# Kernel tuning notes

Measured on AMD Instinct MI355X. Metric: run time of the kernel, lower is better.

The kernel has to match this reference:

```python
import jax, jax.numpy as jnp
import numpy as np

B, T, C = 8, 1024, 1024
H, HKV = 16, 4
HD = C // H            # 64
G = H // HKV           # 4 (GQA group size)
CAP = 50.0
THETA = 10000.0
EPS = 1e-6


def _rope_tables(t, d, theta):
    inv_freq = 1.0 / (theta ** (jnp.arange(0, d, 2, dtype=jnp.float32) / d))
    pos = jnp.arange(t, dtype=jnp.float32)
    freqs = jnp.outer(pos, inv_freq)            # [T, d/2]
    return jnp.cos(freqs), jnp.sin(freqs)


def _rmsnorm(x, w):
    var = jnp.mean(x * x, axis=-1, keepdims=True)
    return x * jax.lax.rsqrt(var + EPS) * w


def _apply_rope(x, cos, sin):
    # x: [B, T, h, HD]; cos/sin: [T, HD/2]
    d = x.shape[-1] // 2
    x1, x2 = x[..., :d], x[..., d:]
    c = cos[None, :, None, :]
    s = sin[None, :, None, :]
    return jnp.concatenate([x1 * c + x2 * s, -x1 * s + x2 * c], axis=-1)


def setup_inputs() -> dict:
    key = jax.random.key(0)
    ks = jax.random.split(key, 6)
    std = 0.02
    x = jax.random.normal(ks[0], (B, T, C), dtype=jnp.float32)
    w_q = jax.random.normal(ks[1], (C, C), dtype=jnp.float32) * std
    w_kv = jax.random.normal(ks[2], (2 * C // G, C), dtype=jnp.float32) * std  # [512, 1024]
    w_c = jax.random.normal(ks[3], (C, C), dtype=jnp.float32) * std
    q_norm_w = jnp.ones((HD,), dtype=jnp.float32)
    k_norm_w = jnp.ones((HD,), dtype=jnp.float32)
    return {"x": x, "w_q": w_q, "w_kv": w_kv, "w_c": w_c,
            "q_norm_w": q_norm_w, "k_norm_w": k_norm_w}


def reference(x, w_q, w_kv, w_c, q_norm_w, k_norm_w):
    # projections (no bias)
    q = (x @ w_q.T).reshape(B, T, H, HD)
    kv = (x @ w_kv.T).reshape(B, T, 2, HKV, HD)
    k, v = kv[:, :, 0], kv[:, :, 1]            # [B, T, HKV, HD]

    # RMSNorm on q/k heads
    q = _rmsnorm(q, q_norm_w)
    k = _rmsnorm(k, k_norm_w)

    # RoPE (half-split rotation, as in apply_rotary_emb)
    cos, sin = _rope_tables(T, HD, THETA)
    q = _apply_rope(q, cos, sin)
    k = _apply_rope(k, cos, sin)

    # GQA layout: heads grouped over kv heads (equiv to repeat_interleave)
    q = q.transpose(0, 2, 1, 3).reshape(B, HKV, G, T, HD)   # [B, nkv, G, T, HD]
    k = k.transpose(0, 2, 1, 3)                             # [B, nkv, T, HD]
    v = v.transpose(0, 2, 1, 3)

    scale = 1.0 / jnp.sqrt(jnp.float32(HD))
    att = jnp.einsum('bngqd,bnkd->bngqk', q, k) * scale     # [B, nkv, G, T, T]
    att = CAP * jnp.tanh(att / CAP)                          # soft logit cap

    causal = jnp.arange(T)[:, None] >= jnp.arange(T)[None, :]  # [T, T]
    att = jnp.where(causal[None, None, None], att, -jnp.inf)
    att = jax.nn.softmax(att, axis=-1)

    y = jnp.einsum('bngqk,bnkd->bngqd', att, v)             # [B, nkv, G, T, HD]
    y = y.reshape(B, H, T, HD).transpose(0, 2, 1, 3).reshape(B, T, C)
    return y @ w_c.T
```

## Files before the change

kernel.cpp:

```cpp
#include <hip/hip_runtime.h>
#include <math.h>

#define BB 8
#define TT 1024
#define CC 1024
#define HH 16
#define HKV 4
#define HD 64
#define MM (BB*TT)
#define LOG2E 1.4426950408889634f

typedef __attribute__((ext_vector_type(8))) short bf16x8;
typedef __attribute__((ext_vector_type(4))) float f32x4;

__device__ __forceinline__ float b2f(unsigned short x){
    union{unsigned int i; float f;} u; u.i = ((unsigned int)x)<<16; return u.f;
}
__device__ __forceinline__ unsigned short f2b(float f){
    union{float f; unsigned int i;} u; u.f = f;
    unsigned int r = u.i + 0x7fffu + ((u.i>>16)&1u);
    return (unsigned short)(r>>16);
}

#define GLD16(gp, lp) __builtin_amdgcn_global_load_lds( \
    (__attribute__((address_space(1))) void*)(gp), \
    (__attribute__((address_space(3))) void*)(lp), 16, 0, 0)

__global__ __launch_bounds__(256) void cvt_all(const float* __restrict__ x,
                                               const float* __restrict__ w_q,
                                               const float* __restrict__ w_kv,
                                               const float* __restrict__ w_c,
                                               unsigned short* __restrict__ xb,
                                               unsigned short* __restrict__ wqkvb,
                                               unsigned short* __restrict__ wcb){
    int i = blockIdx.x*256 + threadIdx.x;
    const float* src; unsigned short* dst; int off;
    if (i < 2097152)      { src = x;    dst = xb;              off = i; }
    else if (i < 2359296) { src = w_q;  dst = wqkvb;           off = i - 2097152; }
    else if (i < 2490368) { src = w_kv; dst = wqkvb + 1048576; off = i - 2359296; }
    else                  { src = w_c;  dst = wcb;             off = i - 2490368; }
    float4 f = ((const float4*)src)[off];
    ushort4 o;
    o.x = f2b(f.x); o.y = f2b(f.y); o.z = f2b(f.z); o.w = f2b(f.w);
    ((ushort4*)dst)[off] = o;
}

template<int BF16OUT>
__global__ __launch_bounds__(256) void gemm_bt(const unsigned short* __restrict__ A,
                                               const unsigned short* __restrict__ Bt,
                                               void* __restrict__ Cc,
                                               int M, int N, int K){
    __shared__ __align__(16) unsigned short As[128*64];
    __shared__ __align__(16) unsigned short Bs[128*64];
    const int tid  = threadIdx.x;
    const int wid  = tid >> 6;
    const int lane = tid & 63;
    const int wm   = wid >> 1;
    const int wn   = wid & 1;
    const int l16  = lane & 15;
    const int quad = lane >> 4;

    int bm, bn;
    {
        int gx = gridDim.x;
        int p  = blockIdx.y * gx + blockIdx.x;
        int nb = gx * gridDim.y;
        int l  = (p & 7) * (nb >> 3) + (p >> 3);
        bn = (l % gx) * 128;
        bm = (l / gx) * 128;
    }

    const unsigned short* ga[4]; const unsigned short* gb[4];
    char* la[4]; char* lb[4];
    {
        int rbase = tid >> 3, c_lds = tid & 7;
        #pragma unroll
        for (int it = 0; it < 4; ++it){
            int row = it*32 + rbase;
            int cg  = c_lds ^ (row & 7);
            ga[it] = A  + (size_t)(bm+row)*K + cg*8;
            gb[it] = Bt + (size_t)(bn+row)*K + cg*8;
            la[it] = (char*)As + (size_t)(it*256 + tid)*16;
            lb[it] = (char*)Bs + (size_t)(it*256 + tid)*16;
        }
    }

    f32x4 acc[4][4] = {};

    for (int k0 = 0; k0 < K; k0 += 64){
        __syncthreads();
        #pragma unroll
        for (int it = 0; it < 4; ++it){
            GLD16(ga[it] + k0, la[it]);
            GLD16(gb[it] + k0, lb[it]);
        }
        __syncthreads();

        #pragma unroll
        for (int kh = 0; kh < 2; ++kh){
            bf16x8 af[4], bfr[4];
            #pragma unroll
            for (int i = 0; i < 4; ++i){
                int row = wm*64 + i*16 + l16;
                int ch  = (kh*4 + quad) ^ (row & 7);
                af[i] = *(const bf16x8*)(As + row*64 + ch*8);
            }
            #pragma unroll
            for (int j = 0; j < 4; ++j){
                int row = wn*64 + j*16 + l16;
                int ch  = (kh*4 + quad) ^ (row & 7);
                bfr[j] = *(const bf16x8*)(Bs + row*64 + ch*8);
            }
            #pragma unroll
            for (int i = 0; i < 4; ++i)
                #pragma unroll
                for (int j = 0; j < 4; ++j)
                    acc[i][j] = __builtin_amdgcn_mfma_f32_16x16x32_bf16(af[i], bfr[j], acc[i][j], 0, 0, 0);
        }
    }

    #pragma unroll
    for (int i = 0; i < 4; ++i){
        int row0 = wm*64 + i*16 + quad*4;
        #pragma unroll
        for (int j = 0; j < 4; ++j){
            int col = bn + wn*64 + j*16 + l16;
            #pragma unroll
            for (int r = 0; r < 4; ++r){
                if (BF16OUT)
                    ((unsigned short*)Cc)[(size_t)(bm + row0 + r)*N + col] = f2b(acc[i][j][r]);
                else
                    ((float*)Cc)[(size_t)(bm + row0 + r)*N + col] = acc[i][j][r];
            }
        }
    }
}

__global__ __launch_bounds__(256) void norm_rope_k(const unsigned short* __restrict__ QKVb,
                                                   const float* __restrict__ kw,
                                                   unsigned short* __restrict__ ka){
    int row  = blockIdx.x;
    int u    = threadIdx.x >> 6;
    int lane = threadIdx.x & 63;
    int b = row >> 10;
    int t = row & 1023;

    float val = b2f(QKVb[(size_t)row*1536 + 1024 + u*64 + lane]);

    float ss = val*val;
    #pragma unroll
    for (int off = 32; off > 0; off >>= 1) ss += __shfl_xor(ss, off, 64);
    float normed = val * rsqrtf(ss*(1.0f/64.0f) + 1e-6f) * kw[lane];

    int i = lane & 31;
    float freq = (float)t * exp2f(-(float)i * (13.287712379549449f/32.0f));
    float s, c;
    sincosf(freq, &s, &c);
    float other = __shfl_xor(normed, 32, 64);
    float outv = (lane < 32) ? (normed*c + other*s) : (-other*s + normed*c);

    ka[(((size_t)(b*HKV + u))*TT + t)*HD + lane] = f2b(outv);
}

__global__ __launch_bounds__(256) void vtrans(const unsigned short* __restrict__ QKVb,
                                              unsigned short* __restrict__ vat){
    __shared__ unsigned short tile[64][72];
    const int tid = threadIdx.x;
    const int tblk = blockIdx.x, n = blockIdx.y, b = blockIdx.z;
    #pragma unroll
    for (int it = 0; it < 2; ++it){
        int i = it*256 + tid;
        int r = i >> 3, c = i & 7;
        uint4 v = *(const uint4*)(QKVb + ((size_t)(b*TT + tblk*64 + r))*1536 + 1280 + n*64 + c*8);
        *(uint4*)(&tile[r][c*8]) = v;
    }
    __syncthreads();
    const int d = tid >> 2, tseg = tid & 3;
    unsigned short tmp[16];
    #pragma unroll
    for (int i = 0; i < 16; ++i) tmp[i] = tile[tseg*16 + i][d];
    size_t off = (((size_t)(b*HKV + n))*HD + d)*TT + tblk*64 + tseg*16;
    *(uint4*)(vat + off)     = *(const uint4*)tmp;
    *(uint4*)(vat + off + 8) = *(const uint4*)(tmp + 8);
}

__global__ __launch_bounds__(512, 4) void attn_mfma(const unsigned short* __restrict__ QKVb,
                                                    const unsigned short* __restrict__ ka,
                                                    const unsigned short* __restrict__ vat,
                                                    const float* __restrict__ qw,
                                                    unsigned short* __restrict__ ya){
    __shared__ __align__(16) unsigned short Ks[64*64];
    __shared__ __align__(16) unsigned short Vts[64*64];
    __shared__ __align__(16) unsigned short Ps[8][32*72];

    const int tid = threadIdx.x;
    const int wave = tid >> 6, lane = tid & 63;
    const int l16 = lane & 15, quad = lane >> 4;
    const int n = blockIdx.x, b = blockIdx.y, iz = blockIdx.z;
    const int ib = (iz < 8) ? iz : 23 - iz;
    const int head = wave & 3, sub = wave >> 2;
    const int h = n*4 + head;
    const int R0[2] = { ib*32 + sub*16, (31-ib)*32 + sub*16 };

    bf16x8 qf[2][2];
    {
        float invf[8], rw0[8], rw1[8];
        #pragma unroll
        for (int j = 0; j < 8; ++j){
            int i = quad*8 + j;
            invf[j] = exp2f(-(float)i * (13.287712379549449f/32.0f));
            rw0[j] = qw[i]; rw1[j] = qw[i + 32];
        }
        #pragma unroll
        for (int h2 = 0; h2 < 2; ++h2){
            const int t = R0[h2] + l16;
            const unsigned short* qp = QKVb + ((size_t)(b*TT + t))*1536 + h*64 + quad*8;
            float x0[8], x1[8];
            {
                uint4 a = *(const uint4*)qp;
                uint4 c = *(const uint4*)(qp + 32);
                const unsigned short* pa = (const unsigned short*)&a;
                const unsigned short* pc = (const unsigned short*)&c;
                #pragma unroll
                for (int j = 0; j < 8; ++j){ x0[j] = b2f(pa[j]); x1[j] = b2f(pc[j]); }
            }
            float ss = 0.f;
            #pragma unroll
            for (int j = 0; j < 8; ++j) ss += x0[j]*x0[j] + x1[j]*x1[j];
            ss += __shfl_xor(ss, 16, 64);
            ss += __shfl_xor(ss, 32, 64);
            float rn = rsqrtf(ss*(1.0f/64.0f) + 1e-6f);
            unsigned short o0[8], o1[8];
            #pragma unroll
            for (int j = 0; j < 8; ++j){
                float s, c;
                sincosf((float)t * invf[j], &s, &c);
                float n0 = x0[j]*rn*rw0[j];
                float n1 = x1[j]*rn*rw1[j];
                o0[j] = f2b(n0*c + n1*s);
                o1[j] = f2b(n1*c - n0*s);
            }
            qf[h2][0] = *(const bf16x8*)o0;
            qf[h2][1] = *(const bf16x8*)o1;
        }
    }

    const unsigned short* kbase = ka  + ((size_t)(b*HKV + n))*TT*HD;
    const unsigned short* vbase = vat + ((size_t)(b*HKV + n))*HD*TT;

    const unsigned short* gk; const unsigned short* gv;
    char* lk; char* lv;
    {
        int row = tid >> 3, slot = tid & 7;
        int cg = slot ^ (row & 7);
        gk = kbase + (size_t)row*HD + cg*8;
        gv = vbase + (size_t)row*TT + cg*8;
        lk = (char*)Ks  + (size_t)tid*16;
        lv = (char*)Vts + (size_t)tid*16;
    }

    f32x4 o[2][4] = {};
    f32x4 lacc[2] = {};
    unsigned short* PsW = &Ps[wave][0];

    bf16x8 ones;
    #pragma unroll
    for (int j = 0; j < 8; ++j) ones[j] = (short)0x3f80;

    const float A1 = 0.125f * LOG2E;
    const float B3 = LOG2E / 3840000.0f;
    const int sw = l16 & 7;
    const int ktmax = (1023 - 32*ib) >> 6;

    for (int kt = 0; kt <= ktmax; ++kt){
        const int k0 = kt*64;
        __syncthreads();
        GLD16(gk + (size_t)k0*HD, lk);
        GLD16(gv + k0, lv);
        __syncthreads();

        const bool act0 = (k0 <= R0[0] + 15);
        f32x4 sacc[2][4];
        __builtin_amdgcn_s_setprio(1);
        #pragma unroll
        for (int j = 0; j < 4; ++j){
            const unsigned short* kr = Ks + (j*16 + l16)*64;
            bf16x8 kf0 = *(const bf16x8*)(kr + (quad ^ sw)*8);
            bf16x8 kf1 = *(const bf16x8*)(kr + ((quad+4) ^ sw)*8);
            if (act0){
                f32x4 z = {};
                z = __builtin_amdgcn_mfma_f32_16x16x32_bf16(kf0, qf[0][0], z, 0,0,0);
                sacc[0][j] = __builtin_amdgcn_mfma_f32_16x16x32_bf16(kf1, qf[0][1], z, 0,0,0);
            }
            {
                f32x4 z = {};
                z = __builtin_amdgcn_mfma_f32_16x16x32_bf16(kf0, qf[1][0], z, 0,0,0);
                sacc[1][j] = __builtin_amdgcn_mfma_f32_16x16x32_bf16(kf1, qf[1][1], z, 0,0,0);
            }
        }
        __builtin_amdgcn_s_setprio(0);
        #pragma unroll
        for (int h2 = 0; h2 < 2; ++h2){
            if (h2 == 0 && !act0) continue;
            const int Rb = R0[h2];
            const bool full = (k0 + 63 <= Rb);
            const int qrow = Rb + l16;
            #pragma unroll
            for (int j = 0; j < 4; ++j){
                float pv[4];
                #pragma unroll
                for (int r = 0; r < 4; ++r){
                    float sr = sacc[h2][j][r];
                    float u  = sr*sr;
                    float p  = exp2f(sr * fmaf(u, -B3, A1));
                    if (!full && (k0 + j*16 + quad*4 + r > qrow)) p = 0.f;
                    pv[r] = p;
                }
                unsigned int pk0, pk1;
                asm("v_cvt_pk_bf16_f32 %0, %1, %2" : "=v"(pk0) : "v"(pv[0]), "v"(pv[1]));
                asm("v_cvt_pk_bf16_f32 %0, %1, %2" : "=v"(pk1) : "v"(pv[2]), "v"(pv[3]));
                *(uint2*)(PsW + (h2*16 + l16)*72 + j*16 + quad*4) = make_uint2(pk0, pk1);
            }
        }
        bf16x8 pf[2][2];
        if (act0){
            pf[0][0] = *(const bf16x8*)(PsW + l16*72 + quad*8);
            pf[0][1] = *(const bf16x8*)(PsW + l16*72 + quad*8 + 32);
        }
        pf[1][0] = *(const bf16x8*)(PsW + (16 + l16)*72 + quad*8);
        pf[1][1] = *(const bf16x8*)(PsW + (16 + l16)*72 + quad*8 + 32);
        __builtin_amdgcn_s_setprio(1);
        if (act0){
            lacc[0] = __builtin_amdgcn_mfma_f32_16x16x32_bf16(pf[0][0], ones, lacc[0], 0,0,0);
            lacc[0] = __builtin_amdgcn_mfma_f32_16x16x32_bf16(pf[0][1], ones, lacc[0], 0,0,0);
        }
        lacc[1] = __builtin_amdgcn_mfma_f32_16x16x32_bf16(pf[1][0], ones, lacc[1], 0,0,0);
        lacc[1] = __builtin_amdgcn_mfma_f32_16x16x32_bf16(pf[1][1], ones, lacc[1], 0,0,0);
        #pragma unroll
        for (int jd = 0; jd < 4; ++jd){
            const unsigned short* vr = Vts + (jd*16 + l16)*64;
            bf16x8 vf0 = *(const bf16x8*)(vr + (quad ^ sw)*8);
            bf16x8 vf1 = *(const bf16x8*)(vr + ((quad+4) ^ sw)*8);
            if (act0){
                o[0][jd] = __builtin_amdgcn_mfma_f32_16x16x32_bf16(pf[0][0], vf0, o[0][jd], 0,0,0);
                o[0][jd] = __builtin_amdgcn_mfma_f32_16x16x32_bf16(pf[0][1], vf1, o[0][jd], 0,0,0);
            }
            o[1][jd] = __builtin_amdgcn_mfma_f32_16x16x32_bf16(pf[1][0], vf0, o[1][jd], 0,0,0);
            o[1][jd] = __builtin_amdgcn_mfma_f32_16x16x32_bf16(pf[1][1], vf1, o[1][jd], 0,0,0);
        }
        __builtin_amdgcn_s_setprio(0);
    }

    #pragma unroll
    for (int h2 = 0; h2 < 2; ++h2){
        const int Rb = R0[h2];
        #pragma unroll
        for (int r = 0; r < 4; ++r){
            float linv = __builtin_amdgcn_rcpf(lacc[h2][r]);
            int t = Rb + quad*4 + r;
            #pragma unroll
            for (int jd = 0; jd < 4; ++jd)
                ya[(((size_t)(b*TT + t))*HH + h)*HD + jd*16 + l16] = f2b(o[h2][jd][r]*linv);
        }
    }
}

extern "C" void kernel_launch(void* const* d_in, const int* in_sizes, int n_in,
                              void* d_out, int out_size, void* d_ws, size_t ws_size,
                              hipStream_t stream) {
    const float* x    = (const float*)d_in[0];
    const float* w_q  = (const float*)d_in[1];
    const float* w_kv = (const float*)d_in[2];
    const float* w_c  = (const float*)d_in[3];
    const float* qw   = (const float*)d_in[4];
    const float* kw   = (const float*)d_in[5];
    float* out = (float*)d_out;

    char* ws = (char*)d_ws;
    unsigned short* xb    = (unsigned short*)(ws);
    unsigned short* wqkvb = (unsigned short*)(ws + ((size_t)16<<20));
    unsigned short* wcb   = (unsigned short*)(ws + ((size_t)19<<20));
    unsigned short* QKVb  = (unsigned short*)(ws + ((size_t)21<<20));
    unsigned short* ka    = (unsigned short*)(ws + ((size_t)45<<20));
    unsigned short* vat   = (unsigned short*)(ws + ((size_t)49<<20));
    unsigned short* ya    = (unsigned short*)(ws + ((size_t)53<<20));

    cvt_all<<<dim3(2752512/256), 256, 0, stream>>>(x, w_q, w_kv, w_c, xb, wqkvb, wcb);

    gemm_bt<1><<<dim3(1536/128, MM/128), 256, 0, stream>>>(xb, wqkvb, (void*)QKVb, MM, 1536, CC);

    vtrans<<<dim3(TT/64, HKV, BB), 256, 0, stream>>>(QKVb, vat);

    norm_rope_k<<<dim3(MM), 256, 0, stream>>>(QKVb, kw, ka);

    attn_mfma<<<dim3(HKV, BB, 16), 512, 0, stream>>>(QKVb, ka, vat, qw, ya);

    gemm_bt<0><<<dim3(CC/128, MM/128), 256, 0, stream>>>(ya, wcb, (void*)out, MM, CC, CC);
}
```

Baseline: 210.5 us.

## Double-buffer LDS tiles in GEMM to overlap global loads with MFMA compute

The GEMM kernel now uses two LDS buffers for the A and B tiles. It prefetches the next K-slice with global_load_lds while computing on the current one, and uses explicit vmcnt waits and s_barrier in place of full __syncthreads around each load. The aim is to hide global memory latency behind the MFMA work. The cost is double the LDS footprint (64KB per block), which can lower occupancy, and it relies on vmcnt counting being correct for the async loads.

```diff
diff --git a/kernel.cpp b/kernel.cpp
--- a/kernel.cpp
+++ b/kernel.cpp
@@ -50,8 +50,8 @@
                                                const unsigned short* __restrict__ Bt,
                                                void* __restrict__ Cc,
                                                int M, int N, int K){
-    __shared__ __align__(16) unsigned short As[128*64];
-    __shared__ __align__(16) unsigned short Bs[128*64];
+    __shared__ __align__(16) unsigned short As[2][128*64];
+    __shared__ __align__(16) unsigned short Bs[2][128*64];
     const int tid  = threadIdx.x;
     const int wid  = tid >> 6;
     const int lane = tid & 63;
@@ -80,44 +80,65 @@
             int cg  = c_lds ^ (row & 7);
             ga[it] = A  + (size_t)(bm+row)*K + cg*8;
             gb[it] = Bt + (size_t)(bn+row)*K + cg*8;
-            la[it] = (char*)As + (size_t)(it*256 + tid)*16;
-            lb[it] = (char*)Bs + (size_t)(it*256 + tid)*16;
+            la[it] = (char*)&As[0][0] + (size_t)(it*256 + tid)*16;
+            lb[it] = (char*)&Bs[0][0] + (size_t)(it*256 + tid)*16;
         }
     }
 
     f32x4 acc[4][4] = {};
 
-    for (int k0 = 0; k0 < K; k0 += 64){
-        __syncthreads();
-        #pragma unroll
-        for (int it = 0; it < 4; ++it){
-            GLD16(ga[it] + k0, la[it]);
-            GLD16(gb[it] + k0, lb[it]);
-        }
-        __syncthreads();
-
-        #pragma unroll
-        for (int kh = 0; kh < 2; ++kh){
-            bf16x8 af[4], bfr[4];
-            #pragma unroll
-            for (int i = 0; i < 4; ++i){
-                int row = wm*64 + i*16 + l16;
-                int ch  = (kh*4 + quad) ^ (row & 7);
-                af[i] = *(const bf16x8*)(As + row*64 + ch*8);
-            }
-            #pragma unroll
-            for (int j = 0; j < 4; ++j){
-                int row = wn*64 + j*16 + l16;
-                int ch  = (kh*4 + quad) ^ (row & 7);
-                bfr[j] = *(const bf16x8*)(Bs + row*64 + ch*8);
-            }
-            #pragma unroll
-            for (int i = 0; i < 4; ++i)
-                #pragma unroll
-                for (int j = 0; j < 4; ++j)
-                    acc[i][j] = __builtin_amdgcn_mfma_f32_16x16x32_bf16(af[i], bfr[j], acc[i][j], 0, 0, 0);
-        }
-    }
+#define STAGE(KOFF, BOFF) do { \
+    _Pragma("unroll") \
+    for (int it = 0; it < 4; ++it){ \
+        GLD16(ga[it] + (KOFF), la[it] + (BOFF)); \
+        GLD16(gb[it] + (KOFF), lb[it] + (BOFF)); \
+    } \
+} while(0)
+
+#define COMPUTE(ASB, BSB) do { \
+    const unsigned short* As_ = (ASB); \
+    const unsigned short* Bs_ = (BSB); \
+    _Pragma("unroll") \
+    for (int kh = 0; kh < 2; ++kh){ \
+        bf16x8 af[4], bfr[4]; \
+        _Pragma("unroll") \
+        for (int i = 0; i < 4; ++i){ \
+            int row = wm*64 + i*16 + l16; \
+            int ch  = (kh*4 + quad) ^ (row & 7); \
+            af[i] = *(const bf16x8*)(As_ + row*64 + ch*8); \
+        } \
+        _Pragma("unroll") \
+        for (int j = 0; j < 4; ++j){ \
+            int row = wn*64 + j*16 + l16; \
+            int ch  = (kh*4 + quad) ^ (row & 7); \
+            bfr[j] = *(const bf16x8*)(Bs_ + row*64 + ch*8); \
+        } \
+        _Pragma("unroll") \
+        for (int i = 0; i < 4; ++i) \
+            _Pragma("unroll") \
+            for (int j = 0; j < 4; ++j) \
+                acc[i][j] = __builtin_amdgcn_mfma_f32_16x16x32_bf16(af[i], bfr[j], acc[i][j], 0, 0, 0); \
+    } \
+} while(0)
+
+    STAGE(0, 0);
+    STAGE(64, 16384);
+
+    for (int k0 = 0; k0 < K; k0 += 128){
+        asm volatile("s_waitcnt vmcnt(8)" ::: "memory");
+        __builtin_amdgcn_s_barrier();
+        COMPUTE(&As[0][0], &Bs[0][0]);
+        __builtin_amdgcn_s_barrier();
+        if (k0 + 128 < K) STAGE(k0 + 128, 0);
+        if (k0 + 128 < K) asm volatile("s_waitcnt vmcnt(8)" ::: "memory");
+        else              asm volatile("s_waitcnt vmcnt(0)" ::: "memory");
+        __builtin_amdgcn_s_barrier();
+        COMPUTE(&As[1][0], &Bs[1][0]);
+        __builtin_amdgcn_s_barrier();
+        if (k0 + 192 < K) STAGE(k0 + 192, 16384);
+    }
+#undef STAGE
+#undef COMPUTE
 
     #pragma unroll
     for (int i = 0; i < 4; ++i){
```

New measurement: 215.3 us. 1.02x slower.
